# Performance work log

Hardware: AMD Instinct MI355X
Metric: run time of the kernel (lower is better)

## Reference

```python
import jax, jax.numpy as jnp
import numpy as np

E = 768
H = 8

def setup_inputs() -> dict:
    key = jax.random.key(0)
    ks = jax.random.split(key, 9)
    s = 1.0 / np.sqrt(E)
    x = jax.random.normal(ks[0], (4, 2048, E), dtype=jnp.float32)
    Wq = jax.random.uniform(ks[1], (E, E), jnp.float32, -s, s)
    bq = jax.random.uniform(ks[2], (E,), jnp.float32, -s, s)
    Wk = jax.random.uniform(ks[3], (E, E), jnp.float32, -s, s)
    bk = jax.random.uniform(ks[4], (E,), jnp.float32, -s, s)
    Wv = jax.random.uniform(ks[5], (E, E), jnp.float32, -s, s)
    bv = jax.random.uniform(ks[6], (E,), jnp.float32, -s, s)
    Wo = jax.random.uniform(ks[7], (E, E), jnp.float32, -s, s)
    bo = jax.random.uniform(ks[8], (E,), jnp.float32, -s, s)
    return {"x": x, "Wq": Wq, "bq": bq, "Wk": Wk, "bk": bk, "Wv": Wv, "bv": bv, "Wo": Wo, "bo": bo}

def reference(x, Wq, bq, Wk, bk, Wv, bv, Wo, bo):
    B, N, Emb = x.shape
    d = Emb // H
    # projections (torch Linear: y = x @ W.T + b)
    q = (x @ Wq.T + bq).reshape(B, N, H, d).transpose(0, 2, 1, 3)  # [B,H,N,d]
    k = (x @ Wk.T + bk).reshape(B, N, H, d).transpose(0, 2, 1, 3)
    v = (x @ Wv.T + bv).reshape(B, N, H, d).transpose(0, 2, 1, 3)
    scores = jnp.einsum('bhnd,bhmd->bhnm', q, k) / jnp.sqrt(jnp.float32(d))
    attn = jax.nn.softmax(scores, axis=-1)  # dropout p=0.0 -> identity
    out = jnp.einsum('bhnm,bhmd->bhnd', attn, v)
    out = out.transpose(0, 2, 1, 3).reshape(B, N, Emb)
    return out @ Wo.T + bo
```

## Files before the change

### kernel.cpp

```cpp
#include <hip/hip_runtime.h>


#define E_DIM 768
#define N_HEAD 8
#define D_HEAD 96
#define B_SZ 4
#define N_SEQ 2048
#define BN (B_SZ * N_SEQ)

typedef unsigned short u16;
typedef __attribute__((ext_vector_type(8))) unsigned short u16x8;
typedef __attribute__((ext_vector_type(4))) unsigned short u16x4;
typedef __attribute__((ext_vector_type(8))) short s16x8;
typedef __attribute__((ext_vector_type(4))) float f32x4;

#define SZ_X   ((size_t)BN * E_DIM)
#define SZ_W   ((size_t)E_DIM * E_DIM)
#define SZ_B   ((size_t)E_DIM)
#define N_CONV (SZ_X + 4 * SZ_W + 4 * SZ_B)

__device__ __forceinline__ float bf2f(u16 u) {
    union { unsigned u; float f; } c; c.u = ((unsigned)u) << 16; return c.f;
}
__device__ __forceinline__ u16 f2bf(float f) {
    union { float f; unsigned u; } c; c.f = f;
    unsigned r = c.u + 0x7FFFu + ((c.u >> 16) & 1u);
    return (u16)(r >> 16);
}
__device__ __forceinline__ void gl_lds16(const u16* g, u16* l) {
    __builtin_amdgcn_global_load_lds(
        (const __attribute__((address_space(1))) unsigned int*)g,
        (__attribute__((address_space(3))) unsigned int*)l, 16, 0, 0);
}

__global__ void detect_dtype(const void* __restrict__ x, int* __restrict__ flag) {
    __shared__ int cnt;
    if (threadIdx.x == 0) cnt = 0;
    __syncthreads();
    const u16* p = (const u16*)x;
    u16 u = p[(size_t)threadIdx.x * 2];
    int ef = (u >> 7) & 0xFF;
    int insane = (ef < 96 || ef > 159) ? 1 : 0;
    atomicAdd(&cnt, insane);
    __syncthreads();
    if (threadIdx.x == 0) *flag = (cnt > 128) ? 1 : 0;
}

__global__ __launch_bounds__(256) void convert8(
    const int* __restrict__ flag,
    const void* __restrict__ x,
    const void* __restrict__ wq, const void* __restrict__ wk,
    const void* __restrict__ wv, const void* __restrict__ wo,
    const void* __restrict__ bq, const void* __restrict__ bk,
    const void* __restrict__ bv, const void* __restrict__ bo,
    u16* __restrict__ dst)
{
    size_t i = ((size_t)blockIdx.x * 256 + threadIdx.x) * 8;
    if (i >= N_CONV) return;
    const int f32 = *flag;
    size_t r = i;
    const void* s;
    if (r < SZ_X) { s = x; }
    else { r -= SZ_X;
      if (r < SZ_W) { s = wq; }
      else { r -= SZ_W;
        if (r < SZ_W) { s = wk; }
        else { r -= SZ_W;
          if (r < SZ_W) { s = wv; }
          else { r -= SZ_W;
            if (r < SZ_W) { s = wo; }
            else { r -= SZ_W;
              if (r < SZ_B) { s = bq; }
              else { r -= SZ_B;
                if (r < SZ_B) { s = bk; }
                else { r -= SZ_B;
                  if (r < SZ_B) { s = bv; }
                  else { r -= SZ_B; s = bo; }
                }
              }
            }
          }
        }
      }
    }
    u16x8 o;
    if (f32) {
        float4 a = ((const float4*)((const float*)s + r))[0];
        float4 b = ((const float4*)((const float*)s + r))[1];
        o[0] = f2bf(a.x); o[1] = f2bf(a.y); o[2] = f2bf(a.z); o[3] = f2bf(a.w);
        o[4] = f2bf(b.x); o[5] = f2bf(b.y); o[6] = f2bf(b.z); o[7] = f2bf(b.w);
    } else {
        o = *(const u16x8*)((const u16*)s + r);
    }
    *(u16x8*)(dst + i) = o;
}

#define GBK 32

#define GEMM_KLOOP(Ab, Wb)                                                            \
    for (int kt = 0; kt < E_DIM; kt += GBK) {                                         \
        __syncthreads();                                                              \
        _Pragma("unroll")                                                             \
        for (int i = 0; i < 2; i++) {                                                 \
            int r0 = wave * 32 + i * 16;                                              \
            gl_lds16(Ab + (size_t)(r0 + lrow) * E_DIM + kt + lcs * 8, &As[r0 * GBK]); \
            gl_lds16(Wb + (size_t)(r0 + lrow) * E_DIM + kt + lcs * 8, &Bs[r0 * GBK]); \
        }                                                                             \
        __syncthreads();                                                              \
        s16x8 af[4], bf[4];                                                           \
        _Pragma("unroll")                                                             \
        for (int mi = 0; mi < 4; mi++)                                                \
            af[mi] = *(const s16x8*)&As[(wm * 64 + mi * 16 + l16) * GBK + q4 * 8];    \
        _Pragma("unroll")                                                             \
        for (int ni = 0; ni < 4; ni++)                                                \
            bf[ni] = *(const s16x8*)&Bs[(wn * 64 + ni * 16 + l16) * GBK + q4 * 8];    \
        _Pragma("unroll")                                                             \
        for (int mi = 0; mi < 4; mi++)                                                \
            _Pragma("unroll")                                                         \
            for (int ni = 0; ni < 4; ni++)                                            \
                acc[mi][ni] = __builtin_amdgcn_mfma_f32_16x16x32_bf16(                \
                    af[mi], bf[ni], acc[mi][ni], 0, 0, 0);                            \
    }

__global__ __launch_bounds__(256) void gemm_mfma_qk(
    const u16* __restrict__ A, const u16* __restrict__ W,
    const u16* __restrict__ bias, u16* __restrict__ C)
{
    __shared__ u16 As[128 * GBK];
    __shared__ u16 Bs[128 * GBK];
    __shared__ u16 Cb[32 * 136];
    const int tid = threadIdx.x;
    const int wave = tid >> 6, lane = tid & 63;
    const int q4 = lane >> 4, l16 = lane & 15;
    const int wm = wave & 1, wn = wave >> 1;
    const int bm = blockIdx.x, bn = blockIdx.y;
    const int lrow = lane >> 2, lcs = lane & 3;

    f32x4 acc[4][4];
    #pragma unroll
    for (int i = 0; i < 4; i++)
        #pragma unroll
        for (int j = 0; j < 4; j++) acc[i][j] = (f32x4){0.f, 0.f, 0.f, 0.f};

    const u16* Ab = A + (size_t)(bm * 128) * E_DIM;
    const u16* Wb = W + (size_t)(bn * 128) * E_DIM;
    GEMM_KLOOP(Ab, Wb)

    u16* Cw = C + (size_t)(bn / 6) * SZ_X;
    const int nc0 = (bn % 6) * 128;
    const int row = tid >> 3, seg = (tid & 7) * 16;
    #pragma unroll
    for (int mi = 0; mi < 4; mi++) {
        __syncthreads();
        #pragma unroll
        for (int ni = 0; ni < 4; ni++) {
            int n_l = wn * 64 + ni * 16 + l16;
            float bi = bf2f(bias[bn * 128 + n_l]);
            #pragma unroll
            for (int r = 0; r < 4; r++)
                Cb[(wm * 16 + q4 * 4 + r) * 136 + n_l] = f2bf(acc[mi][ni][r] + bi);
        }
        __syncthreads();
        int mrow = bm * 128 + (row >> 4) * 64 + mi * 16 + (row & 15);
        *(u16x8*)(Cw + (size_t)mrow * E_DIM + nc0 + seg)     = *(const u16x8*)&Cb[row * 136 + seg];
        *(u16x8*)(Cw + (size_t)mrow * E_DIM + nc0 + seg + 8) = *(const u16x8*)&Cb[row * 136 + seg + 8];
    }
}

__global__ __launch_bounds__(256) void gemm_mfma_v(
    const u16* __restrict__ A, const u16* __restrict__ W,
    const u16* __restrict__ bias, u16* __restrict__ Vt)
{
    __shared__ u16 As[128 * GBK];
    __shared__ u16 Bs[128 * GBK];
    __shared__ u16 Cb[128 * 40];
    const int tid = threadIdx.x;
    const int wave = tid >> 6, lane = tid & 63;
    const int q4 = lane >> 4, l16 = lane & 15;
    const int wm = wave & 1, wn = wave >> 1;
    const int bm = blockIdx.x, bn = blockIdx.y;
    const int lrow = lane >> 2, lcs = lane & 3;

    f32x4 acc[4][4];
    #pragma unroll
    for (int i = 0; i < 4; i++)
        #pragma unroll
        for (int j = 0; j < 4; j++) acc[i][j] = (f32x4){0.f, 0.f, 0.f, 0.f};

    const u16* Ab = A + (size_t)(bm * 128) * E_DIM;
    const u16* Wb = W + (size_t)(bn * 128) * E_DIM;
    GEMM_KLOOP(Ab, Wb)

    const int b = bm >> 4;
    const int n_l = tid >> 1, m0 = (tid & 1) * 16;
    const size_t vrow = (size_t)(b * 768 + bn * 128 + n_l);
    #pragma unroll
    for (int mi = 0; mi < 4; mi++) {
        __syncthreads();
        #pragma unroll
        for (int ni = 0; ni < 4; ni++) {
            int nl = wn * 64 + ni * 16 + l16;
            float bi = bf2f(bias[bn * 128 + nl]);
            #pragma unroll
            for (int r = 0; r < 4; r++)
                Cb[nl * 40 + wm * 16 + q4 * 4 + r] = f2bf(acc[mi][ni][r] + bi);
        }
        __syncthreads();
        int seq0 = (bm & 15) * 128 + (tid & 1) * 64 + mi * 16;
        *(u16x8*)(Vt + vrow * N_SEQ + seq0)     = *(const u16x8*)&Cb[n_l * 40 + m0];
        *(u16x8*)(Vt + vrow * N_SEQ + seq0 + 8) = *(const u16x8*)&Cb[n_l * 40 + m0 + 8];
    }
}

__global__ __launch_bounds__(256) void gemm_mfma_out(
    const u16* __restrict__ A, const u16* __restrict__ W,
    const u16* __restrict__ bias, void* __restrict__ C,
    const int* __restrict__ flag)
{
    __shared__ u16 As[128 * GBK];
    __shared__ u16 Bs[128 * GBK];
    __shared__ float Cbf[32 * 132];
    const int tid = threadIdx.x;
    const int wave = tid >> 6, lane = tid & 63;
    const int q4 = lane >> 4, l16 = lane & 15;
    const int wm = wave & 1, wn = wave >> 1;
    const int bm = blockIdx.x, bn = blockIdx.y;
    const int lrow = lane >> 2, lcs = lane & 3;

    f32x4 acc[4][4];
    #pragma unroll
    for (int i = 0; i < 4; i++)
        #pragma unroll
        for (int j = 0; j < 4; j++) acc[i][j] = (f32x4){0.f, 0.f, 0.f, 0.f};

    const u16* Ab = A + (size_t)(bm * 128) * E_DIM;
    const u16* Wb = W + (size_t)(bn * 128) * E_DIM;
    GEMM_KLOOP(Ab, Wb)

    const int f32 = *flag;
    const int row = tid >> 3, seg = (tid & 7) * 16;
    #pragma unroll
    for (int mi = 0; mi < 4; mi++) {
        __syncthreads();
        #pragma unroll
        for (int ni = 0; ni < 4; ni++) {
            int n_l = wn * 64 + ni * 16 + l16;
            float bi = bf2f(bias[bn * 128 + n_l]);
            #pragma unroll
            for (int r = 0; r < 4; r++)
                Cbf[(wm * 16 + q4 * 4 + r) * 132 + n_l] = acc[mi][ni][r] + bi;
        }
        __syncthreads();
        int mrow = bm * 128 + (row >> 4) * 64 + mi * 16 + (row & 15);
        if (f32) {
            #pragma unroll
            for (int c = 0; c < 4; c++)
                *(float4*)((float*)C + (size_t)mrow * E_DIM + bn * 128 + seg + c * 4) =
                    *(const float4*)&Cbf[row * 132 + seg + c * 4];
        } else {
            u16x8 o0, o1;
            #pragma unroll
            for (int c = 0; c < 8; c++) {
                o0[c] = f2bf(Cbf[row * 132 + seg + c]);
                o1[c] = f2bf(Cbf[row * 132 + seg + 8 + c]);
            }
            *(u16x8*)((u16*)C + (size_t)mrow * E_DIM + bn * 128 + seg)     = o0;
            *(u16x8*)((u16*)C + (size_t)mrow * E_DIM + bn * 128 + seg + 8) = o1;
        }
    }
}

#define QT2 128
#define KT 64

__global__ __launch_bounds__(512) void attn_mfma2(
    const u16* __restrict__ Q, const u16* __restrict__ K,
    const u16* __restrict__ Vt, u16* __restrict__ O)
{
    __shared__ u16 Ks[3 * 64 * 32];
    __shared__ u16 Vts[2 * 96 * 32];
    __shared__ u16 Ps[8 * 16 * 72];

    const int tid = threadIdx.x;
    const int wave = tid >> 6, lane = tid & 63;
    const int q4 = lane >> 4, l16 = lane & 15;
    const int swz = (l16 >> 1) & 3;
    const int b = blockIdx.z, h = blockIdx.y, qb = blockIdx.x;

    const float SCL2 = 0.10206207261596577f * 1.4426950408889634f;

    const int qrow = qb * QT2 + wave * 16 + l16;
    const u16* qptr = Q + (size_t)(b * N_SEQ + qrow) * E_DIM + h * D_HEAD;
    s16x8 qf[3];
    #pragma unroll
    for (int ks = 0; ks < 3; ks++) {
        u16x8 raw = *(const u16x8*)(qptr + ks * 32 + q4 * 8);
        #pragma unroll
        for (int j = 0; j < 8; j++)
            qf[ks][j] = (short)f2bf(bf2f(raw[j]) * SCL2);
    }

    f32x4 of[6];
    #pragma unroll
    for (int i = 0; i < 6; i++) of[i] = (f32x4){0.f, 0.f, 0.f, 0.f};
    float l_r[4] = {0.f, 0.f, 0.f, 0.f};

    u16* psw = Ps + wave * 16 * 72;

    for (int kt = 0; kt < N_SEQ; kt += KT) {
        __syncthreads();
        #pragma unroll
        for (int ii = 0; ii < 3; ii++) {
            int t = wave + 8 * ii;
            if (t < 12) {
                int plane = t >> 2, sub = t & 3;
                int cip = sub * 64 + lane;
                int r = cip >> 2;
                int cs2 = (cip & 3) ^ ((r >> 1) & 3);
                gl_lds16(K + (size_t)(b * N_SEQ + kt + r) * E_DIM + h * D_HEAD + plane * 32 + cs2 * 8,
                         &Ks[plane * 2048 + sub * 512]);
            } else {
                int j = t - 12;
                int plane = j / 6, sub = j - plane * 6;
                int cip = sub * 64 + lane;
                int r = cip >> 2;
                int cs2 = (cip & 3) ^ ((r >> 1) & 3);
                gl_lds16(Vt + (size_t)((b * N_HEAD + h) * D_HEAD + r) * N_SEQ + kt + plane * 32 + cs2 * 8,
                         &Vts[plane * 3072 + sub * 512]);
            }
        }
        __syncthreads();

        f32x4 sf[4];
        #pragma unroll
        for (int i = 0; i < 4; i++) sf[i] = (f32x4){0.f, 0.f, 0.f, 0.f};
        #pragma unroll
        for (int nt = 0; nt < 4; nt++)
            #pragma unroll
            for (int ks = 0; ks < 3; ks++) {
                s16x8 bfr = *(const s16x8*)&Ks[ks * 2048 + (nt * 16 + l16) * 32 + ((q4 ^ swz) << 3)];
                sf[nt] = __builtin_amdgcn_mfma_f32_16x16x32_bf16(qf[ks], bfr, sf[nt], 0, 0, 0);
            }

        #pragma unroll
        for (int nt = 0; nt < 4; nt++)
            #pragma unroll
            for (int r = 0; r < 4; r++) {
                float pv = exp2f(sf[nt][r]);
                l_r[r] += pv;
                psw[(q4 * 4 + r) * 72 + nt * 16 + l16] = f2bf(pv);
            }

        #pragma unroll
        for (int ks2 = 0; ks2 < 2; ks2++) {
            s16x8 afr = *(const s16x8*)&psw[l16 * 72 + ks2 * 32 + q4 * 8];
            #pragma unroll
            for (int nt = 0; nt < 6; nt++) {
                s16x8 bfr = *(const s16x8*)&Vts[ks2 * 3072 + (nt * 16 + l16) * 32 + ((q4 ^ swz) << 3)];
                of[nt] = __builtin_amdgcn_mfma_f32_16x16x32_bf16(afr, bfr, of[nt], 0, 0, 0);
            }
        }
    }

    float linv[4];
    #pragma unroll
    for (int r = 0; r < 4; r++) {
        float l = l_r[r];
        #pragma unroll
        for (int off = 1; off < 16; off <<= 1)
            l += __shfl_xor(l, off, 64);
        linv[r] = 1.0f / l;
    }
    u16* optr = O + (size_t)(b * N_SEQ + qb * QT2 + wave * 16) * E_DIM + h * D_HEAD;
    #pragma unroll
    for (int nt = 0; nt < 6; nt++)
        #pragma unroll
        for (int r = 0; r < 4; r++)
            optr[(size_t)(q4 * 4 + r) * E_DIM + nt * 16 + l16] = f2bf(of[nt][r] * linv[r]);
}

extern "C" void kernel_launch(void* const* d_in, const int* in_sizes, int n_in,
                              void* d_out, int out_size, void* d_ws, size_t ws_size,
                              hipStream_t stream) {
    (void)in_sizes; (void)n_in; (void)out_size; (void)ws_size;
    const void* x  = d_in[0];
    const void* Wq = d_in[1]; const void* bq = d_in[2];
    const void* Wk = d_in[3]; const void* bk = d_in[4];
    const void* Wv = d_in[5]; const void* bv = d_in[6];
    const void* Wo = d_in[7]; const void* bo = d_in[8];

    int* flag = (int*)d_ws;
    u16* base = (u16*)d_ws + 8;
    u16* xb  = base;
    u16* wqb = xb  + SZ_X;
    u16* wvb = wqb + 2 * SZ_W;
    u16* wob = wqb + 3 * SZ_W;
    u16* bqb = wob + SZ_W;
    u16* bvb = bqb + 2 * SZ_B;
    u16* bob = bqb + 3 * SZ_B;
    u16* q_ws = bob + SZ_B;
    u16* k_ws = q_ws + SZ_X;
    u16* vt_ws = k_ws + SZ_X;
    u16* o_ws = vt_ws + SZ_X;

    detect_dtype<<<1, 256, 0, stream>>>(x, flag);
    convert8<<<(int)((N_CONV / 8 + 255) / 256), 256, 0, stream>>>(
        flag, x, Wq, Wk, Wv, Wo, bq, bk, bv, bo, base);

    gemm_mfma_qk<<<dim3(BN / 128, 1536 / 128), 256, 0, stream>>>(xb, wqb, bqb, q_ws);
    gemm_mfma_v <<<dim3(BN / 128,  768 / 128), 256, 0, stream>>>(xb, wvb, bvb, vt_ws);

    attn_mfma2<<<dim3(N_SEQ / QT2, N_HEAD, B_SZ), 512, 0, stream>>>(
        q_ws, k_ws, vt_ws, o_ws);

    gemm_mfma_out<<<dim3(BN / 128, E_DIM / 128), 256, 0, stream>>>(
        o_ws, wob, bob, d_out, flag);
}
```

Before: 281.0 us.

## Fuse QKV projection GEMMs and widen K-tile with XOR-swizzled LDS

Merges the separate QK and V projection kernels into one launch over the concatenated weight matrix, branching on the column block for the V-transposed epilogue. The GEMM K-tile is doubled to 64, with an XOR swizzle on LDS column chunks to avoid bank conflicts, and the staging buffer is reused for the epilogue. This cuts launches, halves the barrier count per K step and reduces LDS conflicts, but raises the LDS footprint per block, which may lower occupancy.

```diff
diff --git a/kernel.cpp b/kernel.cpp
--- a/kernel.cpp
+++ b/kernel.cpp
@@ -95,46 +95,54 @@
     *(u16x8*)(dst + i) = o;
 }
 
-#define GBK 32
-
-#define GEMM_KLOOP(Ab, Wb)                                                            \
-    for (int kt = 0; kt < E_DIM; kt += GBK) {                                         \
-        __syncthreads();                                                              \
-        _Pragma("unroll")                                                             \
-        for (int i = 0; i < 2; i++) {                                                 \
-            int r0 = wave * 32 + i * 16;                                              \
-            gl_lds16(Ab + (size_t)(r0 + lrow) * E_DIM + kt + lcs * 8, &As[r0 * GBK]); \
-            gl_lds16(Wb + (size_t)(r0 + lrow) * E_DIM + kt + lcs * 8, &Bs[r0 * GBK]); \
-        }                                                                             \
-        __syncthreads();                                                              \
-        s16x8 af[4], bf[4];                                                           \
-        _Pragma("unroll")                                                             \
-        for (int mi = 0; mi < 4; mi++)                                                \
-            af[mi] = *(const s16x8*)&As[(wm * 64 + mi * 16 + l16) * GBK + q4 * 8];    \
-        _Pragma("unroll")                                                             \
-        for (int ni = 0; ni < 4; ni++)                                                \
-            bf[ni] = *(const s16x8*)&Bs[(wn * 64 + ni * 16 + l16) * GBK + q4 * 8];    \
-        _Pragma("unroll")                                                             \
-        for (int mi = 0; mi < 4; mi++)                                                \
-            _Pragma("unroll")                                                         \
-            for (int ni = 0; ni < 4; ni++)                                            \
-                acc[mi][ni] = __builtin_amdgcn_mfma_f32_16x16x32_bf16(                \
-                    af[mi], bf[ni], acc[mi][ni], 0, 0, 0);                            \
-    }
-
-__global__ __launch_bounds__(256) void gemm_mfma_qk(
+#define GBK 64
+
+#define GEMM_KLOOP(Ab, Wb)                                                           \
+    for (int kt = 0; kt < E_DIM; kt += GBK) {                                        \
+        __syncthreads();                                                             \
+        _Pragma("unroll")                                                            \
+        for (int j = 0; j < 4; j++) {                                                \
+            int t = wave * 4 + j;                                                    \
+            int row = t * 8 + (lane >> 3);                                           \
+            int cl = (lane & 7) ^ ((lane >> 3) & 7);                                 \
+            gl_lds16(Ab + (size_t)row * E_DIM + kt + cl * 8, &As[t * 8 * GBK]);      \
+            gl_lds16(Wb + (size_t)row * E_DIM + kt + cl * 8, &Bs[t * 8 * GBK]);      \
+        }                                                                            \
+        __syncthreads();                                                             \
+        _Pragma("unroll")                                                            \
+        for (int s = 0; s < 2; s++) {                                                \
+            s16x8 af[4], bf[4];                                                      \
+            _Pragma("unroll")                                                        \
+            for (int mi = 0; mi < 4; mi++) {                                         \
+                int row = wm * 64 + mi * 16 + l16;                                   \
+                af[mi] = *(const s16x8*)&As[row * GBK + ((s * 4 + q4) ^ (l16 & 7)) * 8]; \
+            }                                                                        \
+            _Pragma("unroll")                                                        \
+            for (int ni = 0; ni < 4; ni++) {                                         \
+                int row = wn * 64 + ni * 16 + l16;                                   \
+                bf[ni] = *(const s16x8*)&Bs[row * GBK + ((s * 4 + q4) ^ (l16 & 7)) * 8]; \
+            }                                                                        \
+            _Pragma("unroll")                                                        \
+            for (int mi = 0; mi < 4; mi++)                                           \
+                _Pragma("unroll")                                                    \
+                for (int ni = 0; ni < 4; ni++)                                       \
+                    acc[mi][ni] = __builtin_amdgcn_mfma_f32_16x16x32_bf16(           \
+                        af[mi], bf[ni], acc[mi][ni], 0, 0, 0);                       \
+        }                                                                            \
+    }
+
+__global__ __launch_bounds__(256) void gemm_mfma_qkv(
     const u16* __restrict__ A, const u16* __restrict__ W,
-    const u16* __restrict__ bias, u16* __restrict__ C)
+    const u16* __restrict__ bias, u16* __restrict__ C, u16* __restrict__ Vt)
 {
-    __shared__ u16 As[128 * GBK];
-    __shared__ u16 Bs[128 * GBK];
-    __shared__ u16 Cb[32 * 136];
+    __shared__ u16 smem[2 * 128 * GBK];
+    u16* As = smem;
+    u16* Bs = smem + 128 * GBK;
     const int tid = threadIdx.x;
     const int wave = tid >> 6, lane = tid & 63;
     const int q4 = lane >> 4, l16 = lane & 15;
     const int wm = wave & 1, wn = wave >> 1;
     const int bm = blockIdx.x, bn = blockIdx.y;
-    const int lrow = lane >> 2, lcs = lane & 3;
 
     f32x4 acc[4][4];
     #pragma unroll
@@ -146,40 +154,65 @@
     const u16* Wb = W + (size_t)(bn * 128) * E_DIM;
     GEMM_KLOOP(Ab, Wb)
 
-    u16* Cw = C + (size_t)(bn / 6) * SZ_X;
-    const int nc0 = (bn % 6) * 128;
-    const int row = tid >> 3, seg = (tid & 7) * 16;
-    #pragma unroll
-    for (int mi = 0; mi < 4; mi++) {
-        __syncthreads();
-        #pragma unroll
-        for (int ni = 0; ni < 4; ni++) {
-            int n_l = wn * 64 + ni * 16 + l16;
-            float bi = bf2f(bias[bn * 128 + n_l]);
-            #pragma unroll
-            for (int r = 0; r < 4; r++)
-                Cb[(wm * 16 + q4 * 4 + r) * 136 + n_l] = f2bf(acc[mi][ni][r] + bi);
-        }
-        __syncthreads();
-        int mrow = bm * 128 + (row >> 4) * 64 + mi * 16 + (row & 15);
-        *(u16x8*)(Cw + (size_t)mrow * E_DIM + nc0 + seg)     = *(const u16x8*)&Cb[row * 136 + seg];
-        *(u16x8*)(Cw + (size_t)mrow * E_DIM + nc0 + seg + 8) = *(const u16x8*)&Cb[row * 136 + seg + 8];
-    }
-}
-
-__global__ __launch_bounds__(256) void gemm_mfma_v(
+    if (bn < 12) {
+        u16* Cb = smem;
+        u16* Cw = C + (size_t)(bn / 6) * SZ_X;
+        const int nc0 = (bn % 6) * 128;
+        const int row = tid >> 3, seg = (tid & 7) * 16;
+        #pragma unroll
+        for (int mi = 0; mi < 4; mi++) {
+            __syncthreads();
+            #pragma unroll
+            for (int ni = 0; ni < 4; ni++) {
+                int n_l = wn * 64 + ni * 16 + l16;
+                float bi = bf2f(bias[bn * 128 + n_l]);
+                #pragma unroll
+                for (int r = 0; r < 4; r++)
+                    Cb[(wm * 16 + q4 * 4 + r) * 136 + n_l] = f2bf(acc[mi][ni][r] + bi);
+            }
+            __syncthreads();
+            int mrow = bm * 128 + (row >> 4) * 64 + mi * 16 + (row & 15);
+            *(u16x8*)(Cw + (size_t)mrow * E_DIM + nc0 + seg)     = *(const u16x8*)&Cb[row * 136 + seg];
+            *(u16x8*)(Cw + (size_t)mrow * E_DIM + nc0 + seg + 8) = *(const u16x8*)&Cb[row * 136 + seg + 8];
+        }
+    } else {
+        u16* Cb = smem;
+        const int bnv = bn - 12;
+        const int b = bm >> 4;
+        const int n_l = tid >> 1, m0 = (tid & 1) * 16;
+        const size_t vrow = (size_t)(b * 768 + bnv * 128 + n_l);
+        #pragma unroll
+        for (int mi = 0; mi < 4; mi++) {
+            __syncthreads();
+            #pragma unroll
+            for (int ni = 0; ni < 4; ni++) {
+                int nl = wn * 64 + ni * 16 + l16;
+                float bi = bf2f(bias[bn * 128 + nl]);
+                #pragma unroll
+                for (int r = 0; r < 4; r++)
+                    Cb[nl * 40 + wm * 16 + q4 * 4 + r] = f2bf(acc[mi][ni][r] + bi);
+            }
+            __syncthreads();
+            int seq0 = (bm & 15) * 128 + (tid & 1) * 64 + mi * 16;
+            *(u16x8*)(Vt + vrow * N_SEQ + seq0)     = *(const u16x8*)&Cb[n_l * 40 + m0];
+            *(u16x8*)(Vt + vrow * N_SEQ + seq0 + 8) = *(const u16x8*)&Cb[n_l * 40 + m0 + 8];
+        }
+    }
+}
+
+__global__ __launch_bounds__(256) void gemm_mfma_out(
     const u16* __restrict__ A, const u16* __restrict__ W,
-    const u16* __restrict__ bias, u16* __restrict__ Vt)
+    const u16* __restrict__ bias, void* __restrict__ C,
+    const int* __restrict__ flag)
 {
-    __shared__ u16 As[128 * GBK];
-    __shared__ u16 Bs[128 * GBK];
-    __shared__ u16 Cb[128 * 40];
+    __shared__ u16 smem[2 * 128 * GBK];
+    u16* As = smem;
+    u16* Bs = smem + 128 * GBK;
     const int tid = threadIdx.x;
     const int wave = tid >> 6, lane = tid & 63;
     const int q4 = lane >> 4, l16 = lane & 15;
     const int wm = wave & 1, wn = wave >> 1;
     const int bm = blockIdx.x, bn = blockIdx.y;
-    const int lrow = lane >> 2, lcs = lane & 3;
 
     f32x4 acc[4][4];
     #pragma unroll
@@ -191,52 +224,7 @@
     const u16* Wb = W + (size_t)(bn * 128) * E_DIM;
     GEMM_KLOOP(Ab, Wb)
 
-    const int b = bm >> 4;
-    const int n_l = tid >> 1, m0 = (tid & 1) * 16;
-    const size_t vrow = (size_t)(b * 768 + bn * 128 + n_l);
-    #pragma unroll
-    for (int mi = 0; mi < 4; mi++) {
-        __syncthreads();
-        #pragma unroll
-        for (int ni = 0; ni < 4; ni++) {
-            int nl = wn * 64 + ni * 16 + l16;
-            float bi = bf2f(bias[bn * 128 + nl]);
-            #pragma unroll
-            for (int r = 0; r < 4; r++)
-                Cb[nl * 40 + wm * 16 + q4 * 4 + r] = f2bf(acc[mi][ni][r] + bi);
-        }
-        __syncthreads();
-        int seq0 = (bm & 15) * 128 + (tid & 1) * 64 + mi * 16;
-        *(u16x8*)(Vt + vrow * N_SEQ + seq0)     = *(const u16x8*)&Cb[n_l * 40 + m0];
-        *(u16x8*)(Vt + vrow * N_SEQ + seq0 + 8) = *(const u16x8*)&Cb[n_l * 40 + m0 + 8];
-    }
-}
-
-__global__ __launch_bounds__(256) void gemm_mfma_out(
-    const u16* __restrict__ A, const u16* __restrict__ W,
-    const u16* __restrict__ bias, void* __restrict__ C,
-    const int* __restrict__ flag)
-{
-    __shared__ u16 As[128 * GBK];
-    __shared__ u16 Bs[128 * GBK];
-    __shared__ float Cbf[32 * 132];
-    const int tid = threadIdx.x;
-    const int wave = tid >> 6, lane = tid & 63;
-    const int q4 = lane >> 4, l16 = lane & 15;
-    const int wm = wave & 1, wn = wave >> 1;
-    const int bm = blockIdx.x, bn = blockIdx.y;
-    const int lrow = lane >> 2, lcs = lane & 3;
-
-    f32x4 acc[4][4];
-    #pragma unroll
-    for (int i = 0; i < 4; i++)
-        #pragma unroll
-        for (int j = 0; j < 4; j++) acc[i][j] = (f32x4){0.f, 0.f, 0.f, 0.f};
-
-    const u16* Ab = A + (size_t)(bm * 128) * E_DIM;
-    const u16* Wb = W + (size_t)(bn * 128) * E_DIM;
-    GEMM_KLOOP(Ab, Wb)
-
+    float* Cbf = (float*)smem;
     const int f32 = *flag;
     const int row = tid >> 3, seg = (tid & 7) * 16;
     #pragma unroll
@@ -393,10 +381,8 @@
     u16* base = (u16*)d_ws + 8;
     u16* xb  = base;
     u16* wqb = xb  + SZ_X;
-    u16* wvb = wqb + 2 * SZ_W;
     u16* wob = wqb + 3 * SZ_W;
     u16* bqb = wob + SZ_W;
-    u16* bvb = bqb + 2 * SZ_B;
     u16* bob = bqb + 3 * SZ_B;
     u16* q_ws = bob + SZ_B;
     u16* k_ws = q_ws + SZ_X;
@@ -407,8 +393,8 @@
     convert8<<<(int)((N_CONV / 8 + 255) / 256), 256, 0, stream>>>(
         flag, x, Wq, Wk, Wv, Wo, bq, bk, bv, bo, base);
 
-    gemm_mfma_qk<<<dim3(BN / 128, 1536 / 128), 256, 0, stream>>>(xb, wqb, bqb, q_ws);
-    gemm_mfma_v <<<dim3(BN / 128,  768 / 128), 256, 0, stream>>>(xb, wvb, bvb, vt_ws);
+    gemm_mfma_qkv<<<dim3(BN / 128, 2304 / 128), 256, 0, stream>>>(
+        xb, wqb, bqb, q_ws, vt_ws);
 
     attn_mfma2<<<dim3(N_SEQ / QT2, N_HEAD, B_SZ), 512, 0, stream>>>(
         q_ws, k_ws, vt_ws, o_ws);
```

Measured after the change: 268.2 us. 4.5% less time.
